# Performance work log

Hardware: AMD Instinct MI355X
Metric: run time of the kernel (lower is better)

The kernel has to match this reference:

```python
import jax, jax.numpy as jnp
import numpy as np

N, OUT, IN = 16384, 2048, 2048

def setup_inputs() -> dict:
    key = jax.random.key(0)
    k1, k2, k3 = jax.random.split(key, 3)
    input_ = jax.random.normal(k1, (N, IN), dtype=jnp.float32)
    # kaiming normal, fan_in mode: std = sqrt(2/fan_in)
    weight = jax.random.normal(k2, (OUT, IN), dtype=jnp.float32) * np.sqrt(2.0 / IN)
    mask = jax.random.randint(k3, (OUT, IN), 0, 2, dtype=jnp.int32)
    return {"input_": input_, "weight": weight, "mask": mask}

def reference(input_, weight, mask):
    # out = x @ (W * mask)^T  -- mask is a fixed binary expander pattern
    masked_w = weight * mask.astype(weight.dtype)  # [OUT, IN]
    return jnp.matmul(input_, masked_w.T)          # [N, OUT]
```

## Files before the change

kernel.cpp:

```cpp
#include <hip/hip_runtime.h>


#define MDIM 16384
#define NDIM 2048
#define KDIM 2048

#define BM 256
#define BN 256
#define GRID_X ((MDIM / BM) * (NDIM / BN))

using f32x4   = __attribute__((ext_vector_type(4))) float;
using bf16x8  = __attribute__((ext_vector_type(8))) __bf16;
using ushort8 = __attribute__((ext_vector_type(8))) unsigned short;

typedef __attribute__((address_space(3))) const unsigned short* lds_cptr_t;

__device__ __forceinline__ unsigned short f2bf(float f) {
  unsigned int u = __builtin_bit_cast(unsigned int, f);
  u = u + 0x7FFFu + ((u >> 16) & 1u);
  return (unsigned short)(u >> 16);
}


__global__ void convert_input_kernel(const float* __restrict__ in,
                                     unsigned short* __restrict__ out) {
  size_t base = ((size_t)blockIdx.x * blockDim.x + threadIdx.x) * 8;
  float4 a = *reinterpret_cast<const float4*>(in + base);
  float4 b = *reinterpret_cast<const float4*>(in + base + 4);
  ushort8 v;
  v[0] = f2bf(a.x); v[1] = f2bf(a.y); v[2] = f2bf(a.z); v[3] = f2bf(a.w);
  v[4] = f2bf(b.x); v[5] = f2bf(b.y); v[6] = f2bf(b.z); v[7] = f2bf(b.w);
  *reinterpret_cast<ushort8*>(out + base) = v;
}

__global__ void convert_weight_kernel(const float* __restrict__ w,
                                      const int* __restrict__ mk,
                                      unsigned short* __restrict__ out) {
  size_t base = ((size_t)blockIdx.x * blockDim.x + threadIdx.x) * 8;
  float4 a = *reinterpret_cast<const float4*>(w + base);
  float4 b = *reinterpret_cast<const float4*>(w + base + 4);
  int4 m0 = *reinterpret_cast<const int4*>(mk + base);
  int4 m1 = *reinterpret_cast<const int4*>(mk + base + 4);
  ushort8 v;
  v[0] = m0.x ? f2bf(a.x) : (unsigned short)0;
  v[1] = m0.y ? f2bf(a.y) : (unsigned short)0;
  v[2] = m0.z ? f2bf(a.z) : (unsigned short)0;
  v[3] = m0.w ? f2bf(a.w) : (unsigned short)0;
  v[4] = m1.x ? f2bf(b.x) : (unsigned short)0;
  v[5] = m1.y ? f2bf(b.y) : (unsigned short)0;
  v[6] = m1.z ? f2bf(b.z) : (unsigned short)0;
  v[7] = m1.w ? f2bf(b.w) : (unsigned short)0;
  *reinterpret_cast<ushort8*>(out + base) = v;
}


__device__ __forceinline__ f32x4 MF(bf16x8 a, bf16x8 b, f32x4 c) {
  return __builtin_amdgcn_mfma_f32_16x16x32_bf16(a, b, c, 0, 0, 0);
}
#define VMCNT(n) asm volatile("s_waitcnt vmcnt(" #n ")" ::: "memory")
#define LGKM(n)  asm volatile("s_waitcnt lgkmcnt(" #n ")" ::: "memory")
#define DSR(dst, p, off)                                                        \
  asm volatile("ds_read_b128 %0, %1 offset:%2" : "=v"(dst) : "v"(p), "i"(off))

__global__ __launch_bounds__(512, 2) void gemm_ra2(
    const unsigned short* __restrict__ Abf,
    const unsigned short* __restrict__ Bbf,
    float* __restrict__ C) {
  __shared__ __attribute__((aligned(16))) unsigned short Asl[4 * 8192];
  __shared__ __attribute__((aligned(16))) unsigned short Bsl[4 * 8192];

  int bid = blockIdx.x;
  int wgs = (bid & 7) * (GRID_X / 8) + (bid >> 3);
  int tm = wgs >> 3;
  int tn = wgs & 7;
  int row0 = tm * BM, col0 = tn * BN;

  int t = threadIdx.x;
  int lane = t & 63, wid = t >> 6;
  int wr = wid >> 2, wc = wid & 3;
  int fr = lane & 15, fq = lane >> 4;

  int p0 = (wid * 2) * 64 + lane;
  int r0 = p0 >> 2, kc0 = ((p0 & 3) ^ ((r0 >> 1) & 3)) * 8;
  size_t offA0 = (size_t)(row0 + r0) * KDIM + kc0;
  size_t offB0 = (size_t)(col0 + r0) * KDIM + kc0;
  int ldsw0 = (wid * 2) * 512;

  int kxor = (fq ^ ((fr >> 1) & 3)) * 8;
  int aoff = (wr * 128 + fr) * 32 + kxor;
  int boff = (wc * 64 + fr) * 32 + kxor;
  lds_cptr_t aA = ((lds_cptr_t)Asl) + aoff;
  lds_cptr_t aB = ((lds_cptr_t)Bsl) + boff;

  f32x4 acc[8][4];
#pragma unroll
  for (int m = 0; m < 8; ++m)
#pragma unroll
    for (int n = 0; n < 4; ++n) acc[m][n] = f32x4{0.f, 0.f, 0.f, 0.f};

  bf16x8 aP[8], bP[4], aQ[8], bQ[4];

#define SLOT_A(b, kh) (Asl + ((b) * 2 + (kh)) * 8192)
#define SLOT_B(b, kh) (Bsl + ((b) * 2 + (kh)) * 8192)

#define STG(slot, base, o0, ke) do {                                            \
  __builtin_amdgcn_global_load_lds(                                             \
      (const __attribute__((address_space(1))) void*)((base) + (o0) + (ke)),    \
      (__attribute__((address_space(3))) void*)((slot) + ldsw0), 16, 0, 0);     \
  __builtin_amdgcn_global_load_lds(                                             \
      (const __attribute__((address_space(1))) void*)((base) + (o0) + 32768 +   \
                                                      (ke)),                    \
      (__attribute__((address_space(3))) void*)((slot) + ldsw0 + 512), 16, 0,   \
      0);                                                                       \
} while (0)

#define RD12(b, kh, AD, BD) do {                                                \
  DSR(AD[0], aA, ((b) * 2 + (kh)) * 16384 + 0 * 1024);                          \
  DSR(AD[1], aA, ((b) * 2 + (kh)) * 16384 + 1 * 1024);                          \
  DSR(AD[2], aA, ((b) * 2 + (kh)) * 16384 + 2 * 1024);                          \
  DSR(AD[3], aA, ((b) * 2 + (kh)) * 16384 + 3 * 1024);                          \
  DSR(AD[4], aA, ((b) * 2 + (kh)) * 16384 + 4 * 1024);                          \
  DSR(AD[5], aA, ((b) * 2 + (kh)) * 16384 + 5 * 1024);                          \
  DSR(AD[6], aA, ((b) * 2 + (kh)) * 16384 + 6 * 1024);                          \
  DSR(AD[7], aA, ((b) * 2 + (kh)) * 16384 + 7 * 1024);                          \
  DSR(BD[0], aB, ((b) * 2 + (kh)) * 16384 + 0 * 1024);                          \
  DSR(BD[1], aB, ((b) * 2 + (kh)) * 16384 + 1 * 1024);                          \
  DSR(BD[2], aB, ((b) * 2 + (kh)) * 16384 + 2 * 1024);                          \
  DSR(BD[3], aB, ((b) * 2 + (kh)) * 16384 + 3 * 1024);                          \
} while (0)

#define PHASE(rb, rkh, AC, BC, AD, BD, STAGES, WAITS) do {                      \
  STAGES;                                                                       \
  WAITS;                                                                        \
  __builtin_amdgcn_s_barrier();                                                 \
  RD12(rb, rkh, AD, BD);                                                        \
  LGKM(12);                                                                     \
  __builtin_amdgcn_sched_barrier(0);                                            \
  __builtin_amdgcn_s_setprio(1);                                                \
  _Pragma("unroll")                                                             \
  for (int _m = 0; _m < 8; ++_m)                                                \
    _Pragma("unroll")                                                           \
    for (int _n = 0; _n < 4; ++_n)                                              \
      acc[_m][_n] = MF(AC[_m], BC[_n], acc[_m][_n]);                            \
  __builtin_amdgcn_s_setprio(0);                                                \
  __builtin_amdgcn_s_barrier();                                                 \
} while (0)

  STG(SLOT_A(0, 0), Abf, offA0, 0);
  STG(SLOT_B(0, 0), Bbf, offB0, 0);
  STG(SLOT_A(0, 1), Abf, offA0, 32);
  STG(SLOT_B(0, 1), Bbf, offB0, 32);
  STG(SLOT_A(1, 0), Abf, offA0, 64);
  STG(SLOT_B(1, 0), Bbf, offB0, 64);
  VMCNT(8);
  __builtin_amdgcn_s_barrier();
  RD12(0, 0, aP, bP);

  for (int i = 0; i < 15; ++i) {
    int kb = i * 128;
    PHASE(0, 1, aP, bP, aQ, bQ, { STG(SLOT_A(1, 1), Abf, offA0, kb + 96);
                                  STG(SLOT_B(1, 1), Bbf, offB0, kb + 96); },
          VMCNT(8));
    PHASE(1, 0, aQ, bQ, aP, bP, { STG(SLOT_A(0, 0), Abf, offA0, kb + 128);
                                  STG(SLOT_B(0, 0), Bbf, offB0, kb + 128); },
          VMCNT(8));
    PHASE(1, 1, aP, bP, aQ, bQ, { STG(SLOT_A(0, 1), Abf, offA0, kb + 160);
                                  STG(SLOT_B(0, 1), Bbf, offB0, kb + 160); },
          VMCNT(8));
    PHASE(0, 0, aQ, bQ, aP, bP, { STG(SLOT_A(1, 0), Abf, offA0, kb + 192);
                                  STG(SLOT_B(1, 0), Bbf, offB0, kb + 192); },
          VMCNT(8));
  }
  PHASE(0, 1, aP, bP, aQ, bQ, { STG(SLOT_A(1, 1), Abf, offA0, 2016);
                                STG(SLOT_B(1, 1), Bbf, offB0, 2016); },
        VMCNT(8));
  PHASE(1, 0, aQ, bQ, aP, bP, , VMCNT(4));
  PHASE(1, 1, aP, bP, aQ, bQ, , VMCNT(0));
  {
    LGKM(0);
    __builtin_amdgcn_sched_barrier(0);
#pragma unroll
    for (int m = 0; m < 8; ++m)
#pragma unroll
      for (int n = 0; n < 4; ++n)
        acc[m][n] = MF(aQ[m], bQ[n], acc[m][n]);
  }

  size_t crow = (size_t)(row0 + wr * 128 + fq * 4);
  int ccol = col0 + wc * 64 + fr;
#pragma unroll
  for (int m = 0; m < 8; ++m)
#pragma unroll
    for (int n = 0; n < 4; ++n) {
      float* cp = C + (crow + m * 16) * NDIM + ccol + n * 16;
#pragma unroll
      for (int e = 0; e < 4; ++e) cp[(size_t)e * NDIM] = acc[m][n][e];
    }
#undef PHASE
#undef RD12
#undef STG
#undef SLOT_A
#undef SLOT_B
}


__global__ __launch_bounds__(256) void gemm_fused_fallback(
    const float* __restrict__ Afp,
    const float* __restrict__ Wfp,
    const int* __restrict__ Mk,
    float* __restrict__ C) {
  __shared__ unsigned short As[128 * 32];
  __shared__ unsigned short Bs[128 * 32];
  int bid = blockIdx.x;
  int nwg = (MDIM / 128) * (NDIM / 128);
  int wg = (bid & 7) * (nwg / 8) + (bid >> 3);
  int tm = wg >> 4, tn = wg & 15;
  int row0 = tm * 128, col0 = tn * 128;
  int t = threadIdx.x;
  int lane = t & 63, wv = t >> 6;
  int wr = wv >> 1, wc = wv & 1;
  int fr = lane & 15, fq = lane >> 4;
  f32x4 acc[4][4];
#pragma unroll
  for (int i = 0; i < 4; ++i)
#pragma unroll
    for (int j = 0; j < 4; ++j) acc[i][j] = f32x4{0.f, 0.f, 0.f, 0.f};
  for (int kt = 0; kt < KDIM; kt += 32) {
#pragma unroll
    for (int j = 0; j < 2; ++j) {
      int c = j * 256 + t;
      int r = c >> 2;
      int ko = (c & 3) * 8;
      const float* ga = Afp + (size_t)(row0 + r) * KDIM + kt + ko;
      float4 a0 = *reinterpret_cast<const float4*>(ga);
      float4 a1 = *reinterpret_cast<const float4*>(ga + 4);
      ushort8 va;
      va[0] = f2bf(a0.x); va[1] = f2bf(a0.y); va[2] = f2bf(a0.z); va[3] = f2bf(a0.w);
      va[4] = f2bf(a1.x); va[5] = f2bf(a1.y); va[6] = f2bf(a1.z); va[7] = f2bf(a1.w);
      *reinterpret_cast<ushort8*>(As + (size_t)c * 8) = va;
      const float* gw = Wfp + (size_t)(col0 + r) * KDIM + kt + ko;
      const int* gm = Mk + (size_t)(col0 + r) * KDIM + kt + ko;
      float4 w0 = *reinterpret_cast<const float4*>(gw);
      float4 w1 = *reinterpret_cast<const float4*>(gw + 4);
      int4 m0 = *reinterpret_cast<const int4*>(gm);
      int4 m1 = *reinterpret_cast<const int4*>(gm + 4);
      ushort8 vb;
      vb[0] = m0.x ? f2bf(w0.x) : (unsigned short)0;
      vb[1] = m0.y ? f2bf(w0.y) : (unsigned short)0;
      vb[2] = m0.z ? f2bf(w0.z) : (unsigned short)0;
      vb[3] = m0.w ? f2bf(w0.w) : (unsigned short)0;
      vb[4] = m1.x ? f2bf(w1.x) : (unsigned short)0;
      vb[5] = m1.y ? f2bf(w1.y) : (unsigned short)0;
      vb[6] = m1.z ? f2bf(w1.z) : (unsigned short)0;
      vb[7] = m1.w ? f2bf(w1.w) : (unsigned short)0;
      *reinterpret_cast<ushort8*>(Bs + (size_t)c * 8) = vb;
    }
    __syncthreads();
    bf16x8 af[4], bfr[4];
#pragma unroll
    for (int m2 = 0; m2 < 4; ++m2)
      af[m2] = *reinterpret_cast<const bf16x8*>(As + (wr * 64 + m2 * 16 + fr) * 32 + fq * 8);
#pragma unroll
    for (int n2 = 0; n2 < 4; ++n2)
      bfr[n2] = *reinterpret_cast<const bf16x8*>(Bs + (wc * 64 + n2 * 16 + fr) * 32 + fq * 8);
#pragma unroll
    for (int m2 = 0; m2 < 4; ++m2)
#pragma unroll
      for (int n2 = 0; n2 < 4; ++n2)
        acc[m2][n2] = MF(af[m2], bfr[n2], acc[m2][n2]);
    __syncthreads();
  }
#pragma unroll
  for (int m2 = 0; m2 < 4; ++m2)
#pragma unroll
    for (int n2 = 0; n2 < 4; ++n2) {
      size_t r0 = (size_t)(row0 + wr * 64 + m2 * 16 + fq * 4);
      size_t c0 = (size_t)(col0 + wc * 64 + n2 * 16 + fr);
#pragma unroll
      for (int i = 0; i < 4; ++i) C[(r0 + i) * NDIM + c0] = acc[m2][n2][i];
    }
}


extern "C" void kernel_launch(void* const* d_in, const int* in_sizes, int n_in,
                              void* d_out, int out_size, void* d_ws, size_t ws_size,
                              hipStream_t stream) {
  const float* input  = (const float*)d_in[0];
  const float* weight = (const float*)d_in[1];
  const int*   mask   = (const int*)d_in[2];
  float* out = (float*)d_out;

  const size_t needA = (size_t)MDIM * KDIM * sizeof(unsigned short);
  const size_t needB = (size_t)NDIM * KDIM * sizeof(unsigned short);

  if (ws_size >= needA + needB) {
    unsigned short* Abf = (unsigned short*)d_ws;
    unsigned short* Bbf = (unsigned short*)((char*)d_ws + needA);
    convert_input_kernel<<<(MDIM * (size_t)KDIM / 8) / 256, 256, 0, stream>>>(input, Abf);
    convert_weight_kernel<<<(NDIM * (size_t)KDIM / 8) / 256, 256, 0, stream>>>(weight, mask, Bbf);
    gemm_ra2<<<GRID_X, 512, 0, stream>>>(Abf, Bbf, out);
  } else {
    int nwg = (MDIM / 128) * (NDIM / 128);
    gemm_fused_fallback<<<nwg, 256, 0, stream>>>(input, weight, mask, out);
  }
}
```

Before: 183.7 us.

## Restructure GEMM main loop into two-k-half super-phases with interleaved LDS reloads

The K loop changes from four barrier-separated phases per iteration to two super-phases. Each super-phase stages two k-halves of A and B and computes both register sets. Each A fragment is reloaded from LDS right after its MFMA row finishes, using an in-place tied-operand ds_read, so LDS reads overlap with the MFMAs. This cuts the barrier count in half and spreads LDS traffic across the compute. In exchange it waits on a full vmcnt(0) and lgkmcnt(0) at every super-phase, which shortens the effective global prefetch slack.

Result: faster. 169.1 us (-8.0%).

```diff
diff --git a/kernel.cpp b/kernel.cpp
--- a/kernel.cpp
+++ b/kernel.cpp
@@ -61,8 +61,11 @@
 #define LGKM(n)  asm volatile("s_waitcnt lgkmcnt(" #n ")" ::: "memory")
 #define DSR(dst, p, off)                                                        \
   asm volatile("ds_read_b128 %0, %1 offset:%2" : "=v"(dst) : "v"(p), "i"(off))
-
-__global__ __launch_bounds__(512, 2) void gemm_ra2(
+#define DSRI(dst, p, off)                                                       \
+  asm volatile("ds_read_b128 %0, %1 offset:%2"                                  \
+               : "=v"(dst) : "v"(p), "i"(off), "0"(dst))
+
+__global__ __launch_bounds__(512, 2) void gemm_sp(
     const unsigned short* __restrict__ Abf,
     const unsigned short* __restrict__ Bbf,
     float* __restrict__ C) {
@@ -129,21 +132,43 @@
   DSR(BD[3], aB, ((b) * 2 + (kh)) * 16384 + 3 * 1024);                          \
 } while (0)
 
-#define PHASE(rb, rkh, AC, BC, AD, BD, STAGES, WAITS) do {                      \
-  STAGES;                                                                       \
-  WAITS;                                                                        \
-  __builtin_amdgcn_s_barrier();                                                 \
-  RD12(rb, rkh, AD, BD);                                                        \
-  LGKM(12);                                                                     \
-  __builtin_amdgcn_sched_barrier(0);                                            \
-  __builtin_amdgcn_s_setprio(1);                                                \
+#define MSTEP(mm, AC, BC, sbase) do {                                           \
+  _Pragma("unroll")                                                             \
+  for (int _n = 0; _n < 4; ++_n)                                                \
+    acc[mm][_n] = MF(AC[mm], BC[_n], acc[mm][_n]);                              \
+  DSRI(AC[mm], aA, (sbase) + (mm) * 1024);                                      \
+} while (0)
+
+#define KH(AC, BC, sbase) do {                                                  \
+  MSTEP(0, AC, BC, sbase); MSTEP(1, AC, BC, sbase);                             \
+  MSTEP(2, AC, BC, sbase); MSTEP(3, AC, BC, sbase);                             \
+  MSTEP(4, AC, BC, sbase); MSTEP(5, AC, BC, sbase);                             \
+  MSTEP(6, AC, BC, sbase); MSTEP(7, AC, BC, sbase);                             \
+  DSRI(BC[0], aB, (sbase) + 0 * 1024);                                          \
+  DSRI(BC[1], aB, (sbase) + 1 * 1024);                                          \
+  DSRI(BC[2], aB, (sbase) + 2 * 1024);                                          \
+  DSRI(BC[3], aB, (sbase) + 3 * 1024);                                          \
+} while (0)
+
+#define KHN(AC, BC) do {                                                        \
   _Pragma("unroll")                                                             \
   for (int _m = 0; _m < 8; ++_m)                                                \
     _Pragma("unroll")                                                           \
     for (int _n = 0; _n < 4; ++_n)                                              \
       acc[_m][_n] = MF(AC[_m], BC[_n], acc[_m][_n]);                            \
+} while (0)
+
+#define SUPER(b, rb, STAGES) do {                                               \
+  VMCNT(0);                                                                     \
+  LGKM(0);                                                                      \
+  __builtin_amdgcn_s_barrier();                                                 \
+  __builtin_amdgcn_sched_barrier(0);                                            \
+  STAGES;                                                                       \
+  __builtin_amdgcn_sched_barrier(0);                                            \
+  __builtin_amdgcn_s_setprio(1);                                                \
+  KH(aP, bP, ((rb) * 2 + 0) * 16384);                                           \
+  KH(aQ, bQ, ((rb) * 2 + 1) * 16384);                                           \
   __builtin_amdgcn_s_setprio(0);                                                \
-  __builtin_amdgcn_s_barrier();                                                 \
 } while (0)
 
   STG(SLOT_A(0, 0), Abf, offA0, 0);
@@ -152,38 +177,30 @@
   STG(SLOT_B(0, 1), Bbf, offB0, 32);
   STG(SLOT_A(1, 0), Abf, offA0, 64);
   STG(SLOT_B(1, 0), Bbf, offB0, 64);
+  STG(SLOT_A(1, 1), Abf, offA0, 96);
+  STG(SLOT_B(1, 1), Bbf, offB0, 96);
   VMCNT(8);
   __builtin_amdgcn_s_barrier();
   RD12(0, 0, aP, bP);
+  RD12(0, 1, aQ, bQ);
 
   for (int i = 0; i < 15; ++i) {
     int kb = i * 128;
-    PHASE(0, 1, aP, bP, aQ, bQ, { STG(SLOT_A(1, 1), Abf, offA0, kb + 96);
-                                  STG(SLOT_B(1, 1), Bbf, offB0, kb + 96); },
-          VMCNT(8));
-    PHASE(1, 0, aQ, bQ, aP, bP, { STG(SLOT_A(0, 0), Abf, offA0, kb + 128);
-                                  STG(SLOT_B(0, 0), Bbf, offB0, kb + 128); },
-          VMCNT(8));
-    PHASE(1, 1, aP, bP, aQ, bQ, { STG(SLOT_A(0, 1), Abf, offA0, kb + 160);
-                                  STG(SLOT_B(0, 1), Bbf, offB0, kb + 160); },
-          VMCNT(8));
-    PHASE(0, 0, aQ, bQ, aP, bP, { STG(SLOT_A(1, 0), Abf, offA0, kb + 192);
-                                  STG(SLOT_B(1, 0), Bbf, offB0, kb + 192); },
-          VMCNT(8));
+    SUPER(0, 1, { STG(SLOT_A(0, 0), Abf, offA0, kb + 128);
+                  STG(SLOT_B(0, 0), Bbf, offB0, kb + 128);
+                  STG(SLOT_A(0, 1), Abf, offA0, kb + 160);
+                  STG(SLOT_B(0, 1), Bbf, offB0, kb + 160); });
+    SUPER(1, 0, { STG(SLOT_A(1, 0), Abf, offA0, kb + 192);
+                  STG(SLOT_B(1, 0), Bbf, offB0, kb + 192);
+                  STG(SLOT_A(1, 1), Abf, offA0, kb + 224);
+                  STG(SLOT_B(1, 1), Bbf, offB0, kb + 224); });
   }
-  PHASE(0, 1, aP, bP, aQ, bQ, { STG(SLOT_A(1, 1), Abf, offA0, 2016);
-                                STG(SLOT_B(1, 1), Bbf, offB0, 2016); },
-        VMCNT(8));
-  PHASE(1, 0, aQ, bQ, aP, bP, , VMCNT(4));
-  PHASE(1, 1, aP, bP, aQ, bQ, , VMCNT(0));
+  SUPER(0, 1, );
   {
     LGKM(0);
     __builtin_amdgcn_sched_barrier(0);
-#pragma unroll
-    for (int m = 0; m < 8; ++m)
-#pragma unroll
-      for (int n = 0; n < 4; ++n)
-        acc[m][n] = MF(aQ[m], bQ[n], acc[m][n]);
+    KHN(aP, bP);
+    KHN(aQ, bQ);
   }
 
   size_t crow = (size_t)(row0 + wr * 128 + fq * 4);
@@ -196,7 +213,10 @@
 #pragma unroll
       for (int e = 0; e < 4; ++e) cp[(size_t)e * NDIM] = acc[m][n][e];
     }
-#undef PHASE
+#undef SUPER
+#undef KHN
+#undef KH
+#undef MSTEP
 #undef RD12
 #undef STG
 #undef SLOT_A
@@ -298,7 +318,7 @@
     unsigned short* Bbf = (unsigned short*)((char*)d_ws + needA);
     convert_input_kernel<<<(MDIM * (size_t)KDIM / 8) / 256, 256, 0, stream>>>(input, Abf);
     convert_weight_kernel<<<(NDIM * (size_t)KDIM / 8) / 256, 256, 0, stream>>>(weight, mask, Bbf);
-    gemm_ra2<<<GRID_X, 512, 0, stream>>>(Abf, Bbf, out);
+    gemm_sp<<<GRID_X, 512, 0, stream>>>(Abf, Bbf, out);
   } else {
     int nwg = (MDIM / 128) * (NDIM / 128);
     gemm_fused_fallback<<<nwg, 256, 0, stream>>>(input, weight, mask, out);
```
